# Performance work log

Hardware: AMD Instinct MI355X
Metric: run time of the kernel (lower is better)

The kernel has to match this reference:

```python
import jax, jax.numpy as jnp
import numpy as np

HID = 128
N_BLOCKS = 50000
ATOMS_PER_BLOCK = 8
N_ATOMS = N_BLOCKS * ATOMS_PER_BLOCK  # 400k
N_EDGES = 800000
ATOM_VOCAB = 100
N_BOND_TYPES = 5
CORRUPT_RATIO = 0.1


def setup_inputs() -> dict:
    key = jax.random.key(0)
    ks = jax.random.split(key, 20)
    A = jax.random.randint(ks[0], (N_ATOMS,), 0, ATOM_VOCAB)
    src = jax.random.randint(ks[1], (N_EDGES,), 0, N_ATOMS)
    dst = jax.random.randint(ks[2], (N_EDGES,), 0, N_ATOMS)
    btyp = jax.random.randint(ks[3], (N_EDGES,), 0, N_BOND_TYPES)
    bonds = jnp.stack([src, dst, btyp], axis=1)  # [E, 3]
    block_ids = jnp.arange(N_ATOMS) // ATOMS_PER_BLOCK  # atom -> block, sorted
    generate_mask = jax.random.uniform(ks[4], (N_BLOCKS,)) < 0.5
    position_ids = jax.random.randint(ks[5], (N_BLOCKS,), 0, 1024)
    is_aa = jax.random.randint(ks[6], (N_BLOCKS,), 0, 2)
    corrupt_rand = jax.random.uniform(ks[7], (N_BLOCKS,))
    s = 0.02
    p = {
        'atom_embed': jax.random.normal(ks[8], (ATOM_VOCAB, HID)) * s,
        'bond_embed': jax.random.normal(ks[9], (N_BOND_TYPES, HID)) * s,
        'is_aa_embed': jax.random.normal(ks[10], (2, HID)) * s,
        'gine_w1': jax.random.normal(ks[11], (HID, HID)) * s,
        'gine_b1': jnp.zeros((HID,)),
        'gine_w2': jax.random.normal(ks[12], (HID, HID)) * s,
        'gine_b2': jnp.zeros((HID,)),
        'mlp_w0': jax.random.normal(ks[13], (3 * HID, HID)) * s,
        'mlp_b0': jnp.zeros((HID,)),
        'mlp_w1': jax.random.normal(ks[14], (HID, HID)) * s,
        'mlp_b1': jnp.zeros((HID,)),
        'mlp_w2': jax.random.normal(ks[15], (HID, HID)) * s,
        'mlp_b2': jnp.zeros((HID,)),
    }
    return dict(A=A, bonds=bonds, block_ids=block_ids, generate_mask=generate_mask,
                position_ids=position_ids, is_aa=is_aa, corrupt_rand=corrupt_rand, **p)


def _sinusoidal(pos, dim):
    # standard sinusoidal position embedding, [N] -> [N, dim]
    inv_freq = 1.0 / (10000.0 ** (jnp.arange(0, dim, 2, dtype=jnp.float32) / dim))
    ang = pos.astype(jnp.float32)[:, None] * inv_freq[None, :]
    return jnp.concatenate([jnp.sin(ang), jnp.cos(ang)], axis=-1)


def reference(A, bonds, block_ids, generate_mask, position_ids, is_aa, corrupt_rand,
              atom_embed, bond_embed, is_aa_embed,
              gine_w1, gine_b1, gine_w2, gine_b2,
              mlp_w0, mlp_b0, mlp_w1, mlp_b1, mlp_w2, mlp_b2):
    src, dst, btyp = bonds[:, 0], bonds[:, 1], bonds[:, 2]
    # context atoms: atoms whose block is NOT being generated
    ctx = ~generate_mask[block_ids]                       # [N_atoms]
    valid = (ctx[src] & ctx[dst]).astype(jnp.float32)     # edge-select mask (== dropping bonds)
    # GINEConv: msg = relu(x_j + e), aggregated by sum at dst, eps = 0
    Hn = atom_embed[A]                                    # [N_atoms, H]
    edge_attr = bond_embed[btyp]                          # [E, H]
    msg = jax.nn.relu(Hn[src] + edge_attr) * valid[:, None]
    agg = jax.ops.segment_sum(msg, dst, num_segments=N_ATOMS)
    h = Hn + agg
    h = jax.nn.relu(h @ gine_w1 + gine_b1) @ gine_w2 + gine_b2
    # std-conserving scatter mean: sum / sqrt(count)
    blk_sum = jax.ops.segment_sum(h, block_ids, num_segments=N_BLOCKS)
    cnt = jax.ops.segment_sum(jnp.ones((N_ATOMS,), jnp.float32), block_ids, num_segments=N_BLOCKS)
    topo = blk_sum / jnp.sqrt(jnp.maximum(cnt, 1.0))[:, None]
    topo = jnp.where(generate_mask[:, None], 0.0, topo)
    # is_aa embedding with corruption on generated blocks
    corrupt = generate_mask & (corrupt_rand < CORRUPT_RATIO)
    is_aa_e = is_aa_embed[jnp.where(corrupt, 0, is_aa)]
    pos_e = _sinusoidal(position_ids, HID)
    x = jnp.concatenate([pos_e, topo, is_aa_e], axis=-1)  # [N_blocks, 3H]
    # 3-layer cond MLP (dropout inactive in eval)
    x = jax.nn.relu(x @ mlp_w0 + mlp_b0)
    x = jax.nn.relu(x @ mlp_w1 + mlp_b1)
    cond = x @ mlp_w2 + mlp_b2
    return cond
```

## Files before the change

### kernel.cpp

```cpp
#include <hip/hip_runtime.h>
#include <hip/hip_bf16.h>

#define NBLK  50000
#define NATOM 400000
#define NEDGE 800000
#define CAP   40

typedef __bf16 bf16x8 __attribute__((ext_vector_type(8)));
typedef float  f32x4  __attribute__((ext_vector_type(4)));

#define MCNT_OFF 0UL
#define EW1_OFF  200000UL
#define REC_OFF  251200UL
#define T_OFF    4251200UL
#define PW_OFF   4507200UL
#define W2T_OFF  4769344UL
#define M1T_OFF  4802112UL
#define M2T_OFF  4834880UL
#define AAW_OFF  4867648UL
#define GM_OFF   4869696UL
#define FLAG_OFF 4919696UL
#define TOPO_OFF 4919712UL
#define WS_NEED  18403840UL

#define RS8 0.35355339059327373f

#define MFMA(a,b,c) __builtin_amdgcn_mfma_f32_16x16x32_bf16((a),(b),(c),0,0,0)

__device__ inline f32x4 splat4(float v){ f32x4 r; r[0]=v; r[1]=v; r[2]=v; r[3]=v; return r; }
__device__ inline float scrub(float v){ return (v==v && v<1e30f && v>-1e30f) ? v : 0.f; }

__global__ void k_sniff(const void* gm_raw, char* ws) {
  __shared__ int big;
  if (threadIdx.x == 0) big = 0;
  __syncthreads();
  const unsigned* gw = (const unsigned*)gm_raw;
  for (int i = threadIdx.x; i < 12500; i += 256)
    if (gw[i] > 1u) big = 1;
  __syncthreads();
  if (threadIdx.x == 0) *(int*)(ws + FLAG_OFF) = big;
}

__global__ void k_prep(const float* atom_embed, const float* bond_embed,
                       const float* m0, const float* m1, const float* m2,
                       const float* g2, const float* gb2, const float* aa_embed,
                       const void* gm_raw, char* ws) {
  int b = blockIdx.x, t = threadIdx.x;
  if (b < 100) {
    float ae = atom_embed[b*128 + t];
    float* T = (float*)(ws + T_OFF);
    for (int bo = 0; bo < 5; ++bo) {
      float v = ae + bond_embed[bo*128 + t];
      T[(b*5 + bo)*128 + t] = v > 0.f ? v : 0.f;
    }
  } else if (b < 116) {
    int wb = b - 100;
    const float* src; __bf16* dst; int r0;
    if (wb < 8) { src = m1; dst = (__bf16*)(ws + M1T_OFF); r0 = wb*16; }
    else        { src = m2; dst = (__bf16*)(ws + M2T_OFF); r0 = (wb-8)*16; }
    for (int rr = 0; rr < 16; ++rr) {
      int r = r0 + rr;
      dst[t*128 + r] = (__bf16)src[r*128 + t];
    }
  } else if (b < 166) {
    int anyBig = *(const int*)(ws + FLAG_OFF);
    int base = (b - 116) * 1000;
    unsigned char* gu = (unsigned char*)(ws + GM_OFF);
    if (anyBig) {
      const unsigned char* gb = (const unsigned char*)gm_raw;
      for (int i = t; i < 1000; i += 128) gu[base+i] = gb[base+i] ? 1 : 0;
    } else {
      const int* gi = (const int*)gm_raw;
      for (int i = t; i < 1000; i += 128) gu[base+i] = gi[base+i] ? 1 : 0;
    }
  } else if (b < 1190) {
    int p = b - 166;
    __shared__ float s[128];
    int c = t & 63;
    float invf = exp2f((float)c * -0.20762050593046012f);
    float ang = (float)p * invf;
    s[t] = (t < 64) ? __sinf(ang) : __cosf(ang);
    __syncthreads();
    float acc = 0.f;
    #pragma unroll 4
    for (int j = 0; j < 128; ++j) acc += s[j] * m0[j*128 + t];
    ((__bf16*)(ws + PW_OFF))[p*128 + t] = (__bf16)acc;
  } else if (b < 1318) {
    int r = b - 1190;
    float acc = 0.f;
    #pragma unroll 4
    for (int j = 0; j < 128; ++j) acc += g2[r*128 + j] * m0[(128+j)*128 + t];
    ((__bf16*)(ws + W2T_OFF))[t*128 + r] = (__bf16)(acc * RS8);
  } else {
    int sf = b - 1318, sel = sf & 1, f = sf >> 1;
    float acc = 0.f;
    #pragma unroll 4
    for (int j = 0; j < 128; ++j) acc += aa_embed[sel*128 + j] * m0[(256+j)*128 + t];
    if (f) {
      float cacc = 0.f;
      #pragma unroll 4
      for (int j = 0; j < 128; ++j) cacc += gb2[j] * m0[(128+j)*128 + t];
      acc += 8.0f * RS8 * cacc;
    }
    ((float*)(ws + AAW_OFF))[sf*128 + t] = acc;
  }
}

__global__ void k_prep2(const float* atom_embed, const float* g1, const float* gb1,
                        char* ws) {
  int b = blockIdx.x, t = threadIdx.x;
  float s0 = 0.f, s1 = 0.f, s2 = 0.f, s3 = 0.f;
  const float* row = (b < 100) ? (atom_embed + b*128) : ((float*)(ws + T_OFF) + (b-100)*128);
  #pragma unroll 4
  for (int k = 0; k < 128; k += 4) {
    s0 += row[k+0] * g1[(k+0)*128 + t];
    s1 += row[k+1] * g1[(k+1)*128 + t];
    s2 += row[k+2] * g1[(k+2)*128 + t];
    s3 += row[k+3] * g1[(k+3)*128 + t];
  }
  float s = (s0 + s1) + (s2 + s3);
  if (b < 100) {
    ((float*)(ws + EW1_OFF))[b*128 + t] = s + gb1[t];
  } else {
    __syncthreads();
    ((float*)(ws + T_OFF))[(b-100)*128 + t] = s;
  }
}

__global__ void k_scatter4(const int* __restrict__ bonds, const int* __restrict__ A, char* ws) {
  int base = (blockIdx.x*256 + threadIdx.x)*4;
  if (base >= NEDGE) return;
  const unsigned char* gm = (const unsigned char*)(ws + GM_OFF);
  const int4* bp = (const int4*)(bonds + (long)base*3);
  int4 w0 = bp[0], w1 = bp[1], w2 = bp[2];
  int srcs[4] = {w0.x, w0.w, w1.z, w2.y};
  int dsts[4] = {w0.y, w1.x, w1.w, w2.z};
  int bts[4]  = {w0.z, w1.y, w2.x, w2.w};
  #pragma unroll
  for (int i = 0; i < 4; ++i) {
    if (gm[srcs[i] >> 3] | gm[dsts[i] >> 3]) continue;
    int mol = dsts[i] >> 3;
    int slot = atomicAdd((int*)(ws + MCNT_OFF) + mol, 1);
    if (slot >= 0 && slot < CAP)
      ((unsigned short*)(ws + REC_OFF))[mol*CAP + slot] =
        (unsigned short)((A[srcs[i]]*5 + bts[i])*8 + (dsts[i] & 7));
  }
}

__launch_bounds__(256, 8)
__global__ void k_gather4(char* ws, const int* __restrict__ A) {
  const int tid = threadIdx.x;
  const int lane = tid & 63, wid = tid >> 6;
  const int mol = blockIdx.x*4 + wid;
  const int a_l = lane >> 3, q8 = lane & 7;
  const unsigned char* gm = (const unsigned char*)(ws + GM_OFF);

  f32x4 a0 = splat4(0.f), a1 = splat4(0.f), a2 = splat4(0.f), a3 = splat4(0.f);
  f32x4 b0 = splat4(0.f), b1 = splat4(0.f), b2 = splat4(0.f), b3 = splat4(0.f);
  if (!gm[mol]) {
    const int* cnt = (const int*)(ws + MCNT_OFF);
    const unsigned* rec32 = (const unsigned*)(ws + REC_OFF);
    const unsigned short* rec16 = (const unsigned short*)(ws + REC_OFF);
    const float* EW1 = (const float*)(ws + EW1_OFF);
    const float* TW1 = (const float*)(ws + T_OFF);
    int n = cnt[mol];
    if (n > CAP) n = CAP;
    if (n < 0) n = 0;
    int aT = A[mol*8 + a_l];
    const f32x4* ep = (const f32x4*)(EW1 + aT*128 + q8*16);
    a0 = ep[0]; a1 = ep[1]; a2 = ep[2]; a3 = ep[3];
    const int half = n >> 1;
    const int base32 = mol*(CAP/2);
    for (int i = 0; i < half; ++i) {
      unsigned pr = rec32[base32 + i];
      int rv0 = pr & 0xFFFF, rv1 = pr >> 16;
      int p0 = rv0 >> 3, p1 = rv1 >> 3;
      if (p0 < 500 && (rv0 & 7) == a_l) {
        const f32x4* tp = (const f32x4*)(TW1 + p0*128 + q8*16);
        a0 += tp[0]; a1 += tp[1]; a2 += tp[2]; a3 += tp[3];
      }
      if (p1 < 500 && (rv1 & 7) == a_l) {
        const f32x4* tp = (const f32x4*)(TW1 + p1*128 + q8*16);
        b0 += tp[0]; b1 += tp[1]; b2 += tp[2]; b3 += tp[3];
      }
    }
    if (n & 1) {
      int rv = rec16[mol*CAP + n - 1];
      int p = rv >> 3;
      if (p < 500 && (rv & 7) == a_l) {
        const f32x4* tp = (const f32x4*)(TW1 + p*128 + q8*16);
        b0 += tp[0]; b1 += tp[1]; b2 += tp[2]; b3 += tp[3];
      }
    }
  }
  #pragma unroll
  for (int k = 0; k < 4; ++k) {
    float x0 = fmaxf(a0[k] + b0[k], 0.f), x1 = fmaxf(a1[k] + b1[k], 0.f);
    float x2 = fmaxf(a2[k] + b2[k], 0.f), x3 = fmaxf(a3[k] + b3[k], 0.f);
    x0 += __shfl_xor(x0, 8);  x1 += __shfl_xor(x1, 8);
    x2 += __shfl_xor(x2, 8);  x3 += __shfl_xor(x3, 8);
    x0 += __shfl_xor(x0, 16); x1 += __shfl_xor(x1, 16);
    x2 += __shfl_xor(x2, 16); x3 += __shfl_xor(x3, 16);
    x0 += __shfl_xor(x0, 32); x1 += __shfl_xor(x1, 32);
    x2 += __shfl_xor(x2, 32); x3 += __shfl_xor(x3, 32);
    a0[k] = x0; a1[k] = x1; a2[k] = x2; a3[k] = x3;
  }
  if (a_l == 0) {
    bf16x8 o0, o1;
    #pragma unroll
    for (int k = 0; k < 4; ++k) {
      o0[k] = (__bf16)a0[k]; o0[k+4] = (__bf16)a1[k];
      o1[k] = (__bf16)a2[k]; o1[k+4] = (__bf16)a3[k];
    }
    char* dst = ws + TOPO_OFF + (long)mol*256 + q8*32;
    *(bf16x8*)dst = o0;
    *(bf16x8*)(dst + 16) = o1;
  }
}

__device__ inline void gemm4(const char* sm, int aoff, const __bf16* wt,
                             const float* bias, int lane, int wave, f32x4 acc[4][2]) {
  const int colA = wave*32 + (lane & 15);
  const int k0   = (lane >> 4) * 8;
  float bb0 = bias[colA], bb1 = bias[colA + 16];
  #pragma unroll
  for (int m = 0; m < 4; ++m) { acc[m][0] = splat4(bb0); acc[m][1] = splat4(bb1); }
  #pragma unroll
  for (int kb = 0; kb < 4; ++kb) {
    bf16x8 b0 = *(const bf16x8*)(wt + colA*128 + kb*32 + k0);
    bf16x8 b1 = *(const bf16x8*)(wt + (colA+16)*128 + kb*32 + k0);
    #pragma unroll
    for (int m = 0; m < 4; ++m) {
      int rA = m*16 + (lane & 15);
      int byte = aoff + rA*256 + (((kb*64) + k0*2) ^ ((rA & 7) << 4));
      bf16x8 a = *(const bf16x8*)(sm + byte);
      acc[m][0] = MFMA(a, b0, acc[m][0]);
      acc[m][1] = MFMA(a, b1, acc[m][1]);
    }
  }
}

__device__ inline void stor4(char* sm, int off, f32x4 acc[4][2],
                             int lane, int wave, bool do_relu) {
  #pragma unroll
  for (int m = 0; m < 4; ++m)
  #pragma unroll
  for (int nf = 0; nf < 2; ++nf)
  #pragma unroll
  for (int r = 0; r < 4; ++r) {
    float v = acc[m][nf][r];
    if (do_relu && v < 0.f) v = 0.f;
    int row = m*16 + (lane >> 4)*4 + r;
    int col = wave*32 + nf*16 + (lane & 15);
    int byte = off + row*256 + ((col*2) ^ ((row & 7) << 4));
    *(__bf16*)(sm + byte) = (__bf16)v;
  }
}

__launch_bounds__(256)
__global__ void k_mlp3(char* ws, const int* __restrict__ pos_ids,
                       const int* __restrict__ is_aa, const float* cr,
                       const float* mb0, const float* mb1, const float* mb2,
                       float* __restrict__ out) {
  __shared__ __align__(16) char sm[32768];
  const int tid = threadIdx.x, lane = tid & 63, wave = tid >> 6;
  const int r0 = blockIdx.x * 64;
  const unsigned char* gm = (const unsigned char*)(ws + GM_OFF);
  const __bf16* topo_pre = (const __bf16*)(ws + TOPO_OFF);

  for (int i = 0; i < 4; ++i) {
    int idx = tid + i*256;
    int row = idx >> 4, c = idx & 15;
    int mol = r0 + row;
    bf16x8 v;
    #pragma unroll
    for (int j = 0; j < 8; ++j) v[j] = (__bf16)0.f;
    if (mol < NBLK) v = *(const bf16x8*)(topo_pre + (long)mol*128 + c*8);
    int byte = row*256 + ((c*16) ^ ((row & 7) << 4));
    *(bf16x8*)(sm + byte) = v;
  }
  if (tid < 64) {
    int mol = r0 + tid, packed = 0;
    if (mol < NBLK) {
      int g = gm[mol];
      int corrupt = g && (cr[mol] < 0.1f);
      int sel = corrupt ? 0 : is_aa[mol];
      packed = pos_ids[mol] | (sel << 12) | ((g ? 0 : 1) << 13);
    }
    *(int*)(sm + 16384 + tid*4) = packed;
  }
  __syncthreads();

  f32x4 acc[4][2];
  gemm4(sm, 0, (const __bf16*)(ws + W2T_OFF), mb0, lane, wave, acc);
  {
    const __bf16* PW = (const __bf16*)(ws + PW_OFF);
    const float* AAW = (const float*)(ws + AAW_OFF);
    #pragma unroll
    for (int m = 0; m < 4; ++m)
    #pragma unroll
    for (int r = 0; r < 4; ++r) {
      int row = m*16 + (lane >> 4)*4 + r;
      int packed = *(const int*)(sm + 16384 + row*4);
      int pid = packed & 0xFFF, sf = (packed >> 12) & 3;
      #pragma unroll
      for (int nf = 0; nf < 2; ++nf) {
        int col = wave*32 + nf*16 + (lane & 15);
        float v = acc[m][nf][r] + (float)PW[pid*128 + col] + AAW[sf*128 + col];
        acc[m][nf][r] = fmaxf(v, 0.f);
      }
    }
  }
  __syncthreads();
  stor4(sm, 0, acc, lane, wave, false);
  __syncthreads();

  gemm4(sm, 0, (const __bf16*)(ws + M1T_OFF), mb1, lane, wave, acc);
  stor4(sm, 16384, acc, lane, wave, true);
  __syncthreads();

  gemm4(sm, 16384, (const __bf16*)(ws + M2T_OFF), mb2, lane, wave, acc);
  #pragma unroll
  for (int m = 0; m < 4; ++m)
  #pragma unroll
  for (int nf = 0; nf < 2; ++nf)
  #pragma unroll
  for (int r = 0; r < 4; ++r) {
    int row = m*16 + (lane >> 4)*4 + r;
    int col = wave*32 + nf*16 + (lane & 15);
    int mol = r0 + row;
    if (mol < NBLK) out[(long)mol*128 + col] = scrub(acc[m][nf][r]);
  }
}

extern "C" void kernel_launch(void* const* d_in, const int* in_sizes, int n_in,
                              void* d_out, int out_size, void* d_ws, size_t ws_size,
                              hipStream_t stream) {
  if (ws_size < WS_NEED) return;
  const int* A      = (const int*)d_in[0];
  const int* bonds  = (const int*)d_in[1];
  const void* gm    = d_in[3];
  const int* pos    = (const int*)d_in[4];
  const int* isaa   = (const int*)d_in[5];
  const float* cr   = (const float*)d_in[6];
  const float* atom_embed = (const float*)d_in[7];
  const float* bond_embed = (const float*)d_in[8];
  const float* aa_embed   = (const float*)d_in[9];
  const float* g1  = (const float*)d_in[10];
  const float* gb1 = (const float*)d_in[11];
  const float* g2  = (const float*)d_in[12];
  const float* gb2 = (const float*)d_in[13];
  const float* m0  = (const float*)d_in[14];
  const float* mb0 = (const float*)d_in[15];
  const float* m1  = (const float*)d_in[16];
  const float* mb1 = (const float*)d_in[17];
  const float* m2  = (const float*)d_in[18];
  const float* mb2 = (const float*)d_in[19];
  char* ws = (char*)d_ws;

  hipMemsetAsync(ws + MCNT_OFF, 0, (size_t)NBLK*4, stream);
  k_sniff   <<<1, 256, 0, stream>>>(gm, ws);
  k_prep    <<<1322, 128, 0, stream>>>(atom_embed, bond_embed, m0, m1, m2,
                                       g2, gb2, aa_embed, gm, ws);
  k_scatter4<<<782, 256, 0, stream>>>(bonds, A, ws);
  k_prep2   <<<600, 128, 0, stream>>>(atom_embed, g1, gb1, ws);
  k_gather4 <<<NBLK/4, 256, 0, stream>>>(ws, A);
  k_mlp3    <<<(NBLK + 63)/64, 256, 0, stream>>>(ws, pos, isaa, cr,
                                                 mb0, mb1, mb2, (float*)d_out);
}
```

Measured before the change: 123.6 us.

## Fold edge scatter into prep kernel and unroll gather record loop by four

Removes the separate scatter kernel by appending 782 extra blocks to k_prep that bucket edges by destination molecule, eight edges per thread. The generate-mask lookup now reads the raw mask directly, as bytes or 32-bit words depending on the sniff flag, instead of a staged byte copy in the workspace. The gather kernel processes four records per iteration to expose more independent loads, and its launch bounds drop from 8 to 6 waves, which gives it more registers. This saves one launch and lets scatter overlap with the prep work, at the cost of a heavier mixed-role kernel.

Measured after the change: 113.8 us, median of 2. -7.9%, faster.

```diff
diff --git a/kernel.cpp b/kernel.cpp
--- a/kernel.cpp
+++ b/kernel.cpp
@@ -44,7 +44,8 @@
 __global__ void k_prep(const float* atom_embed, const float* bond_embed,
                        const float* m0, const float* m1, const float* m2,
                        const float* g2, const float* gb2, const float* aa_embed,
-                       const void* gm_raw, char* ws) {
+                       const void* gm_raw, const int* __restrict__ bonds,
+                       const int* __restrict__ A, char* ws) {
   int b = blockIdx.x, t = threadIdx.x;
   if (b < 100) {
     float ae = atom_embed[b*128 + t];
@@ -91,7 +92,7 @@
     #pragma unroll 4
     for (int j = 0; j < 128; ++j) acc += g2[r*128 + j] * m0[(128+j)*128 + t];
     ((__bf16*)(ws + W2T_OFF))[t*128 + r] = (__bf16)(acc * RS8);
-  } else {
+  } else if (b < 1322) {
     int sf = b - 1318, sel = sf & 1, f = sf >> 1;
     float acc = 0.f;
     #pragma unroll 4
@@ -103,6 +104,31 @@
       acc += 8.0f * RS8 * cacc;
     }
     ((float*)(ws + AAW_OFF))[sf*128 + t] = acc;
+  } else {
+    int anyBig = *(const int*)(ws + FLAG_OFF);
+    const unsigned char* g8 = (const unsigned char*)gm_raw;
+    const int* g32 = (const int*)gm_raw;
+    long base = ((long)(b - 1322)*128 + t)*8;
+    #pragma unroll 2
+    for (int h = 0; h < 2; ++h) {
+      long e4 = base + h*4;
+      if (e4 >= NEDGE) break;
+      const int4* bp = (const int4*)(bonds + e4*3);
+      int4 w0 = bp[0], w1 = bp[1], w2 = bp[2];
+      int srcs[4] = {w0.x, w0.w, w1.z, w2.y};
+      int dsts[4] = {w0.y, w1.x, w1.w, w2.z};
+      int bts[4]  = {w0.z, w1.y, w2.x, w2.w};
+      #pragma unroll
+      for (int i = 0; i < 4; ++i) {
+        int sm_ = srcs[i] >> 3, dm = dsts[i] >> 3;
+        int bad = anyBig ? ((int)g8[sm_] | (int)g8[dm]) : (g32[sm_] | g32[dm]);
+        if (bad) continue;
+        int slot = atomicAdd((int*)(ws + MCNT_OFF) + dm, 1);
+        if (slot >= 0 && slot < CAP)
+          ((unsigned short*)(ws + REC_OFF))[dm*CAP + slot] =
+            (unsigned short)((A[srcs[i]]*5 + bts[i])*8 + (dsts[i] & 7));
+      }
+    }
   }
 }
 
@@ -127,28 +153,8 @@
   }
 }
 
-__global__ void k_scatter4(const int* __restrict__ bonds, const int* __restrict__ A, char* ws) {
-  int base = (blockIdx.x*256 + threadIdx.x)*4;
-  if (base >= NEDGE) return;
-  const unsigned char* gm = (const unsigned char*)(ws + GM_OFF);
-  const int4* bp = (const int4*)(bonds + (long)base*3);
-  int4 w0 = bp[0], w1 = bp[1], w2 = bp[2];
-  int srcs[4] = {w0.x, w0.w, w1.z, w2.y};
-  int dsts[4] = {w0.y, w1.x, w1.w, w2.z};
-  int bts[4]  = {w0.z, w1.y, w2.x, w2.w};
-  #pragma unroll
-  for (int i = 0; i < 4; ++i) {
-    if (gm[srcs[i] >> 3] | gm[dsts[i] >> 3]) continue;
-    int mol = dsts[i] >> 3;
-    int slot = atomicAdd((int*)(ws + MCNT_OFF) + mol, 1);
-    if (slot >= 0 && slot < CAP)
-      ((unsigned short*)(ws + REC_OFF))[mol*CAP + slot] =
-        (unsigned short)((A[srcs[i]]*5 + bts[i])*8 + (dsts[i] & 7));
-  }
-}
-
-__launch_bounds__(256, 8)
-__global__ void k_gather4(char* ws, const int* __restrict__ A) {
+__launch_bounds__(256, 6)
+__global__ void k_gather5(char* ws, const int* __restrict__ A) {
   const int tid = threadIdx.x;
   const int lane = tid & 63, wid = tid >> 6;
   const int mol = blockIdx.x*4 + wid;
@@ -169,12 +175,14 @@
     int aT = A[mol*8 + a_l];
     const f32x4* ep = (const f32x4*)(EW1 + aT*128 + q8*16);
     a0 = ep[0]; a1 = ep[1]; a2 = ep[2]; a3 = ep[3];
-    const int half = n >> 1;
     const int base32 = mol*(CAP/2);
-    for (int i = 0; i < half; ++i) {
-      unsigned pr = rec32[base32 + i];
-      int rv0 = pr & 0xFFFF, rv1 = pr >> 16;
-      int p0 = rv0 >> 3, p1 = rv1 >> 3;
+    int i = 0;
+    for (; i + 4 <= n; i += 4) {
+      unsigned pr0 = rec32[base32 + (i >> 1)];
+      unsigned pr1 = rec32[base32 + (i >> 1) + 1];
+      int rv0 = pr0 & 0xFFFF, rv1 = pr0 >> 16;
+      int rv2 = pr1 & 0xFFFF, rv3 = pr1 >> 16;
+      int p0 = rv0 >> 3, p1 = rv1 >> 3, p2 = rv2 >> 3, p3 = rv3 >> 3;
       if (p0 < 500 && (rv0 & 7) == a_l) {
         const f32x4* tp = (const f32x4*)(TW1 + p0*128 + q8*16);
         a0 += tp[0]; a1 += tp[1]; a2 += tp[2]; a3 += tp[3];
@@ -183,9 +191,17 @@
         const f32x4* tp = (const f32x4*)(TW1 + p1*128 + q8*16);
         b0 += tp[0]; b1 += tp[1]; b2 += tp[2]; b3 += tp[3];
       }
-    }
-    if (n & 1) {
-      int rv = rec16[mol*CAP + n - 1];
+      if (p2 < 500 && (rv2 & 7) == a_l) {
+        const f32x4* tp = (const f32x4*)(TW1 + p2*128 + q8*16);
+        a0 += tp[0]; a1 += tp[1]; a2 += tp[2]; a3 += tp[3];
+      }
+      if (p3 < 500 && (rv3 & 7) == a_l) {
+        const f32x4* tp = (const f32x4*)(TW1 + p3*128 + q8*16);
+        b0 += tp[0]; b1 += tp[1]; b2 += tp[2]; b3 += tp[3];
+      }
+    }
+    for (; i < n; ++i) {
+      int rv = rec16[mol*CAP + i];
       int p = rv >> 3;
       if (p < 500 && (rv & 7) == a_l) {
         const f32x4* tp = (const f32x4*)(TW1 + p*128 + q8*16);
@@ -359,12 +375,11 @@
   char* ws = (char*)d_ws;
 
   hipMemsetAsync(ws + MCNT_OFF, 0, (size_t)NBLK*4, stream);
-  k_sniff   <<<1, 256, 0, stream>>>(gm, ws);
-  k_prep    <<<1322, 128, 0, stream>>>(atom_embed, bond_embed, m0, m1, m2,
-                                       g2, gb2, aa_embed, gm, ws);
-  k_scatter4<<<782, 256, 0, stream>>>(bonds, A, ws);
-  k_prep2   <<<600, 128, 0, stream>>>(atom_embed, g1, gb1, ws);
-  k_gather4 <<<NBLK/4, 256, 0, stream>>>(ws, A);
-  k_mlp3    <<<(NBLK + 63)/64, 256, 0, stream>>>(ws, pos, isaa, cr,
-                                                 mb0, mb1, mb2, (float*)d_out);
-}
+  k_sniff  <<<1, 256, 0, stream>>>(gm, ws);
+  k_prep   <<<2104, 128, 0, stream>>>(atom_embed, bond_embed, m0, m1, m2,
+                                      g2, gb2, aa_embed, gm, bonds, A, ws);
+  k_prep2  <<<600, 128, 0, stream>>>(atom_embed, g1, gb1, ws);
+  k_gather5<<<NBLK/4, 256, 0, stream>>>(ws, A);
+  k_mlp3   <<<(NBLK + 63)/64, 256, 0, stream>>>(ws, pos, isaa, cr,
+                                                mb0, mb1, mb2, (float*)d_out);
+}
```
